# Optimization experiments

Measured on AMD Instinct MI355X. Metric: run time of the kernel, lower is better.

The kernel has to match this reference:

```python
import jax, jax.numpy as jnp
import numpy as np

N = 10000
E = 320000
DIM_IN, DIM_H, DIM_OUT, HEADS = 256, 64, 32, 8
NEG_SLOPE = 0.2


def setup_inputs() -> dict:
    key = jax.random.key(0)
    ks = jax.random.split(key, 10)
    x = jax.random.normal(ks[0], (N, DIM_IN), dtype=jnp.float32)
    edge_index = jax.random.randint(ks[1], (2, E), 0, N, dtype=jnp.int64)
    def glorot(k, shape, fan_in):
        return jax.random.normal(k, shape, dtype=jnp.float32) / np.sqrt(fan_in)
    # layer 1: GATv2Conv(256 -> 64, heads=8)
    W1l = glorot(ks[2], (DIM_IN, HEADS * DIM_H), DIM_IN)
    W1r = glorot(ks[3], (DIM_IN, HEADS * DIM_H), DIM_IN)
    att1 = glorot(ks[4], (HEADS, DIM_H), DIM_H)
    b1 = jnp.zeros((HEADS * DIM_H,), dtype=jnp.float32)
    # layer 2: GATv2Conv(512 -> 32, heads=1)
    W2l = glorot(ks[5], (HEADS * DIM_H, DIM_OUT), HEADS * DIM_H)
    W2r = glorot(ks[6], (HEADS * DIM_H, DIM_OUT), HEADS * DIM_H)
    att2 = glorot(ks[7], (1, DIM_OUT), DIM_OUT)
    b2 = jnp.zeros((DIM_OUT,), dtype=jnp.float32)
    return {"x": x, "edge_index": edge_index, "W1l": W1l, "W1r": W1r,
            "att1": att1, "b1": b1, "W2l": W2l, "W2r": W2r, "att2": att2, "b2": b2}


def gatv2_conv(x, src, dst, Wl, Wr, att, bias, heads, out_ch, concat):
    n = x.shape[0]
    xl = (x @ Wl).reshape(n, heads, out_ch)  # source transform
    xr = (x @ Wr).reshape(n, heads, out_ch)  # target transform
    e = jax.nn.leaky_relu(xl[src] + xr[dst], NEG_SLOPE)       # [E,H,C]
    alpha = jnp.einsum('ehc,hc->eh', e, att)                  # [E,H]
    amax = jax.lax.stop_gradient(
        jax.ops.segment_max(alpha, dst, num_segments=n))      # [N,H]
    ex = jnp.exp(alpha - amax[dst])
    denom = jax.ops.segment_sum(ex, dst, num_segments=n)
    alpha = ex / (denom[dst] + 1e-16)
    msg = xl[src] * alpha[..., None]                          # [E,H,C]
    out = jax.ops.segment_sum(msg, dst, num_segments=n)       # [N,H,C]
    out = out.reshape(n, heads * out_ch) if concat else out.mean(axis=1)
    return out + bias


def reference(x, edge_index, W1l, W1r, att1, b1, W2l, W2r, att2, b2):
    n = x.shape[0]
    loops = jnp.arange(n, dtype=edge_index.dtype)
    src = jnp.concatenate([edge_index[0], loops])  # add_self_loops=True (PyG default)
    dst = jnp.concatenate([edge_index[1], loops])
    h = gatv2_conv(x, src, dst, W1l, W1r, att1, b1, HEADS, DIM_H, True)
    h = jax.nn.elu(h)
    h = gatv2_conv(h, src, dst, W2l, W2r, att2, b2, 1, DIM_OUT, True)
    return jax.nn.log_softmax(h, axis=1)
```

## Files before the change

### kernel.cpp

```cpp
#include <hip/hip_runtime.h>
#include <hip/hip_bf16.h>


constexpr int N_NODES = 10000;
constexpr int N_EDGES = 320000;
constexpr int ET      = N_EDGES + N_NODES;
constexpr float NEG_SLOPE = 0.2f;

constexpr int NB_COUNT  = (ET + 255) / 256;
constexpr int NB_CONVX  = (N_NODES * 64) / 256;
constexpr int NB_CONVW  = (1024 * 64) / 256;
constexpr int NB_CONVW2 = (64 * 128) / 256;

typedef __attribute__((ext_vector_type(8))) short short8;
typedef __attribute__((ext_vector_type(8))) unsigned short ushort8_t;
typedef __attribute__((ext_vector_type(4))) float floatx4;

__device__ __forceinline__ float lrelu(float a) {
    return fmaxf(a, NEG_SLOPE * a);
}
__device__ __forceinline__ unsigned short f2bf(float f) {
    unsigned u = __float_as_uint(f);
    unsigned r = u + 0x7FFFu + ((u >> 16) & 1u);
    return (unsigned short)(r >> 16);
}
__device__ __forceinline__ float bf2f(unsigned short h) {
    return __uint_as_float((unsigned)h << 16);
}
__device__ __forceinline__ float red8_dpp(float p) {
    int x;
    x = __builtin_amdgcn_update_dpp(0, __float_as_int(p), 0xB1, 0xF, 0xF, true);
    p += __int_as_float(x);
    x = __builtin_amdgcn_update_dpp(0, __float_as_int(p), 0x4E, 0xF, 0xF, true);
    p += __int_as_float(x);
    x = __builtin_amdgcn_update_dpp(0, __float_as_int(p), 0x141, 0xF, 0xF, true);
    p += __int_as_float(x);
    return p;
}
__device__ __forceinline__ float red8max_dpp(float p) {
    int x;
    x = __builtin_amdgcn_update_dpp(0, __float_as_int(p), 0xB1, 0xF, 0xF, true);
    p = fmaxf(p, __int_as_float(x));
    x = __builtin_amdgcn_update_dpp(0, __float_as_int(p), 0x4E, 0xF, 0xF, true);
    p = fmaxf(p, __int_as_float(x));
    x = __builtin_amdgcn_update_dpp(0, __float_as_int(p), 0x141, 0xF, 0xF, true);
    p = fmaxf(p, __int_as_float(x));
    return p;
}
__device__ __forceinline__ float ror8_add(float p) {
    int x = __builtin_amdgcn_update_dpp(0, __float_as_int(p), 0x128, 0xF, 0xF, true);
    return p + __int_as_float(x);
}


__global__ __launch_bounds__(256) void k_prep(const int* __restrict__ ei,
        int* __restrict__ deg, const float* __restrict__ x,
        unsigned short* __restrict__ A, const float* __restrict__ Wl,
        const float* __restrict__ Wr, unsigned short* __restrict__ Bt,
        const float* __restrict__ W2l, const float* __restrict__ W2r,
        unsigned short* __restrict__ Bt2) {
    int b = blockIdx.x, t = threadIdx.x;
    if (b < NB_COUNT) {
        int e = b * 256 + t;
        if (e >= ET) return;
        int d = (e < N_EDGES) ? ei[N_EDGES + e] : (e - N_EDGES);
        atomicAdd(&deg[d], 1);
    } else if (b < NB_COUNT + NB_CONVX) {
        int idx = (b - NB_COUNT) * 256 + t;
        int m = idx >> 6, kg = (idx & 63) << 2;
        float4 v = *reinterpret_cast<const float4*>(x + (size_t)m * 256 + kg);
        ushort4 hi = make_ushort4(f2bf(v.x), f2bf(v.y), f2bf(v.z), f2bf(v.w));
        *reinterpret_cast<ushort4*>(A + (size_t)m * 256 + kg) = hi;
    } else if (b < NB_COUNT + NB_CONVX + NB_CONVW) {
        int idx = (b - NB_COUNT - NB_CONVX) * 256 + t;
        int n = idx >> 6, kg = (idx & 63) << 2;
        const float* src = (n < 512) ? (Wl + n) : (Wr + (n - 512));
        float v0 = src[(size_t)(kg + 0) * 512];
        float v1 = src[(size_t)(kg + 1) * 512];
        float v2 = src[(size_t)(kg + 2) * 512];
        float v3 = src[(size_t)(kg + 3) * 512];
        ushort4 hi = make_ushort4(f2bf(v0), f2bf(v1), f2bf(v2), f2bf(v3));
        *reinterpret_cast<ushort4*>(Bt + (size_t)n * 256 + kg) = hi;
    } else {
        int idx = (b - NB_COUNT - NB_CONVX - NB_CONVW) * 256 + t;
        int j = idx >> 7, kg = (idx & 127) << 2;
        const float* src = (j < 32) ? (W2l + j) : (W2r + (j - 32));
        float v0 = src[(size_t)(kg + 0) * 32];
        float v1 = src[(size_t)(kg + 1) * 32];
        float v2 = src[(size_t)(kg + 2) * 32];
        float v3 = src[(size_t)(kg + 3) * 32];
        ushort4 hi = make_ushort4(f2bf(v0), f2bf(v1), f2bf(v2), f2bf(v3));
        *reinterpret_cast<ushort4*>(Bt2 + (size_t)j * 512 + kg) = hi;
    }
}


__global__ __launch_bounds__(1024) void k_scan(const int* __restrict__ deg,
                                               int* __restrict__ offs) {
    __shared__ int part[1024];
    const int CH = 10;
    int t = threadIdx.x;
    int base = t * CH;
    int loc[CH];
    int s = 0;
    for (int i = 0; i < CH; ++i) {
        int idx = base + i;
        int v = (idx < N_NODES) ? deg[idx] : 0;
        loc[i] = s; s += v;
    }
    part[t] = s;
    __syncthreads();
    for (int o = 1; o < 1024; o <<= 1) {
        int add = (t >= o) ? part[t - o] : 0;
        __syncthreads();
        part[t] += add;
        __syncthreads();
    }
    int excl = part[t] - s;
    for (int i = 0; i < CH; ++i) {
        int idx = base + i;
        if (idx < N_NODES) offs[idx] = excl + loc[i];
    }
    if (t == 1023) offs[N_NODES] = part[1023];
}

__global__ void k_scatter(const int* __restrict__ ei, const int* __restrict__ offs,
                          int* __restrict__ deg, int* __restrict__ ssrc) {
    int e = blockIdx.x * 256 + threadIdx.x;
    if (e >= ET) return;
    int s, d;
    if (e < N_EDGES) { s = ei[e]; d = ei[N_EDGES + e]; }
    else             { s = d = e - N_EDGES; }
    int pos = offs[d] + atomicAdd(&deg[d], -1) - 1;
    ssrc[pos] = s;
}


__global__ __launch_bounds__(256) void k_mfma1(const unsigned short* __restrict__ A,
        const unsigned short* __restrict__ Bt, unsigned short* __restrict__ xl1b,
        unsigned short* __restrict__ xr1b) {
    __shared__ unsigned short As[128 * 40];
    __shared__ unsigned short Bs[128 * 40];
    int t = threadIdx.x;
    int wave = t >> 6, L = t & 63;
    int wm = wave & 1, wn = wave >> 1;
    int row0 = blockIdx.x * 128, n0 = blockIdx.y * 128;
    int q = L >> 4, rr = L & 15;
    floatx4 acc[4][4];
#pragma unroll
    for (int i = 0; i < 4; ++i)
#pragma unroll
        for (int j = 0; j < 4; ++j) acc[i][j] = (floatx4){0.f, 0.f, 0.f, 0.f};
    int ra = t >> 2,        ka = (t & 3) * 8;
    int rb = (t + 256) >> 2, kb = ((t + 256) & 3) * 8;
    int gma = row0 + ra; gma = (gma < N_NODES) ? gma : (N_NODES - 1);
    int gmb = row0 + rb; gmb = (gmb < N_NODES) ? gmb : (N_NODES - 1);
    for (int kc = 0; kc < 256; kc += 32) {
        __syncthreads();
        *reinterpret_cast<uint4*>(&As[ra * 40 + ka]) =
            *reinterpret_cast<const uint4*>(A + (size_t)gma * 256 + kc + ka);
        *reinterpret_cast<uint4*>(&As[rb * 40 + kb]) =
            *reinterpret_cast<const uint4*>(A + (size_t)gmb * 256 + kc + kb);
        *reinterpret_cast<uint4*>(&Bs[ra * 40 + ka]) =
            *reinterpret_cast<const uint4*>(Bt + (size_t)(n0 + ra) * 256 + kc + ka);
        *reinterpret_cast<uint4*>(&Bs[rb * 40 + kb]) =
            *reinterpret_cast<const uint4*>(Bt + (size_t)(n0 + rb) * 256 + kc + kb);
        __syncthreads();
        short8 af[4], bf[4];
#pragma unroll
        for (int st = 0; st < 4; ++st)
            af[st] = *reinterpret_cast<const short8*>(
                &As[(wm * 64 + st * 16 + rr) * 40 + q * 8]);
#pragma unroll
        for (int st = 0; st < 4; ++st)
            bf[st] = *reinterpret_cast<const short8*>(
                &Bs[(wn * 64 + st * 16 + rr) * 40 + q * 8]);
#pragma unroll
        for (int i = 0; i < 4; ++i)
#pragma unroll
            for (int j = 0; j < 4; ++j)
                acc[i][j] = __builtin_amdgcn_mfma_f32_16x16x32_bf16(
                    af[i], bf[j], acc[i][j], 0, 0, 0);
    }
#pragma unroll
    for (int j = 0; j < 4; ++j) {
        int gc = n0 + wn * 64 + j * 16 + rr;
        unsigned short* dst = (gc < 512) ? xl1b : xr1b;
        int col = (gc < 512) ? gc : (gc - 512);
#pragma unroll
        for (int i = 0; i < 4; ++i)
#pragma unroll
            for (int r = 0; r < 4; ++r) {
                int gr = row0 + wm * 64 + i * 16 + q * 4 + r;
                if (gr < N_NODES)
                    dst[(size_t)gr * 512 + col] = f2bf(acc[i][j][r]);
            }
    }
}

__global__ __launch_bounds__(256) void k_node1f(const int* __restrict__ offs,
        const int* __restrict__ ssrc, const unsigned short* __restrict__ xl1b,
        const unsigned short* __restrict__ xr1b, const float* __restrict__ att1,
        const float* __restrict__ b1, unsigned short* __restrict__ h1b) {
    int t = threadIdx.x;
    int wave = t >> 6, lane = t & 63;
    int n = blockIdx.x * 4 + wave;
    if (n >= N_NODES) return;
    int beg = offs[n], dcnt = offs[n + 1] - beg;
    float xrv[8], atv[8];
    {
        ushort8_t xru = *reinterpret_cast<const ushort8_t*>(
            xr1b + (size_t)n * 512 + lane * 8);
        const float* atrow = att1 + lane * 8;
        float4 c0 = *reinterpret_cast<const float4*>(atrow);
        float4 c1 = *reinterpret_cast<const float4*>(atrow + 4);
#pragma unroll
        for (int i = 0; i < 8; ++i) xrv[i] = bf2f(xru[i]);
        atv[0]=c0.x; atv[1]=c0.y; atv[2]=c0.z; atv[3]=c0.w;
        atv[4]=c1.x; atv[5]=c1.y; atv[6]=c1.z; atv[7]=c1.w;
    }
    float l = 0.f;
    float acc8[8];
#pragma unroll
    for (int i = 0; i < 8; ++i) acc8[i] = 0.f;
    const int* sp = ssrc + beg;
    const char* xlbase = reinterpret_cast<const char*>(xl1b) + lane * 16;
    auto ld_row = [&](int off) -> ushort8_t {
        return *reinterpret_cast<const ushort8_t*>(xlbase + off);
    };
    for (int b0 = 0; b0 < dcnt; b0 += 64) {
        int bn = dcnt - b0; if (bn > 64) bn = 64;
        int idxv = sp[b0 + ((lane < bn) ? lane : (bn - 1))];
        auto off_at = [&](int k) -> int {
            int kc = (k < bn) ? k : (bn - 1);
            return __shfl(idxv, kc, 64) << 10;
        };
        auto edge = [&](ushort8_t u, int idx) {
            float xs[8];
#pragma unroll
            for (int j = 0; j < 8; ++j) xs[j] = bf2f(u[j]);
            float p0 = 0.f, p1 = 0.f;
#pragma unroll
            for (int j = 0; j < 4; ++j) {
                p0 += lrelu(xs[j] + xrv[j]) * atv[j];
                p1 += lrelu(xs[j + 4] + xrv[j + 4]) * atv[j + 4];
            }
            float p = red8_dpp(p0 + p1);
            float w = __expf(fminf(p, 60.f));
            if (idx >= bn) w = 0.f;
            l += w;
#pragma unroll
            for (int j = 0; j < 8; ++j) acc8[j] += w * xs[j];
        };
        ushort8_t u0 = ld_row(off_at(0));
        ushort8_t u1 = ld_row(off_at(1));
        ushort8_t u2 = ld_row(off_at(2));
        ushort8_t u3 = ld_row(off_at(3));
        for (int i = 0; i < bn; i += 4) {
            ushort8_t n0 = ld_row(off_at(i + 4));
            ushort8_t n1 = ld_row(off_at(i + 5));
            ushort8_t n2 = ld_row(off_at(i + 6));
            ushort8_t n3 = ld_row(off_at(i + 7));
            edge(u0, i);
            edge(u1, i + 1);
            edge(u2, i + 2);
            edge(u3, i + 3);
            u0 = n0; u1 = n1; u2 = n2; u3 = n3;
        }
    }
    float inv = 1.f / (l + 1e-16f);
    const float* brow = b1 + lane * 8;
    ushort8_t vout;
#pragma unroll
    for (int j = 0; j < 8; ++j) {
        float v = acc8[j] * inv + brow[j];
        v = (v > 0.f) ? v : (__expf(v) - 1.f);
        vout[j] = f2bf(v);
    }
    *reinterpret_cast<ushort8_t*>(h1b + (size_t)n * 512 + lane * 8) = vout;
}


__global__ __launch_bounds__(256) void k_mfma2(const unsigned short* __restrict__ h1b,
        const unsigned short* __restrict__ Bt2, float* __restrict__ xw2) {
    __shared__ unsigned short Hs[64 * 40];
    __shared__ unsigned short Ws[64 * 40];
    int t = threadIdx.x;
    int wave = t >> 6, L = t & 63;
    int row0 = blockIdx.x * 64;
    int q = L >> 4, rr = L & 15;
    floatx4 acc[4];
#pragma unroll
    for (int j = 0; j < 4; ++j) acc[j] = (floatx4){0.f, 0.f, 0.f, 0.f};
    int ra = t >> 2, ka = (t & 3) * 8;
    int gma = row0 + ra; gma = (gma < N_NODES) ? gma : (N_NODES - 1);
    for (int kc = 0; kc < 512; kc += 32) {
        __syncthreads();
        *reinterpret_cast<uint4*>(&Hs[ra * 40 + ka]) =
            *reinterpret_cast<const uint4*>(h1b + (size_t)gma * 512 + kc + ka);
        *reinterpret_cast<uint4*>(&Ws[ra * 40 + ka]) =
            *reinterpret_cast<const uint4*>(Bt2 + (size_t)ra * 512 + kc + ka);
        __syncthreads();
        short8 af = *reinterpret_cast<const short8*>(
            &Hs[(wave * 16 + rr) * 40 + q * 8]);
#pragma unroll
        for (int j = 0; j < 4; ++j) {
            short8 bf = *reinterpret_cast<const short8*>(
                &Ws[(j * 16 + rr) * 40 + q * 8]);
            acc[j] = __builtin_amdgcn_mfma_f32_16x16x32_bf16(af, bf, acc[j], 0, 0, 0);
        }
    }
#pragma unroll
    for (int j = 0; j < 4; ++j) {
        int gc = j * 16 + rr;
#pragma unroll
        for (int r = 0; r < 4; ++r) {
            int gr = row0 + wave * 16 + q * 4 + r;
            if (gr < N_NODES) xw2[(size_t)gr * 64 + gc] = acc[j][r];
        }
    }
}

__global__ __launch_bounds__(256) void k_node2f(const int* __restrict__ offs,
        const int* __restrict__ ssrc, const float* __restrict__ xw2,
        const float* __restrict__ att2, const float* __restrict__ b2,
        float* __restrict__ out) {
    int t = threadIdx.x;
    int wave = t >> 6, lane = t & 63;
    int n = blockIdx.x * 4 + wave;
    if (n >= N_NODES) return;
    int ej = lane >> 3;
    int cg = lane & 7;
    int beg = offs[n], dcnt = offs[n + 1] - beg;
    float4 xr = *reinterpret_cast<const float4*>(
                    xw2 + (size_t)n * 64 + 32 + cg * 4);
    float4 at = *reinterpret_cast<const float4*>(att2 + cg * 4);
    float l = 0.f;
    float4 ac = {0.f, 0.f, 0.f, 0.f};
    const int* sp = ssrc + beg;
    const char* xwbase = reinterpret_cast<const char*>(xw2) + cg * 16;
    auto ld_off = [&](int i1) -> int {
        int i1c = (i1 < dcnt) ? i1 : (dcnt - 1);
        return sp[i1c] << 8;
    };
    auto ld_row = [&](int off) -> float4 {
        return *reinterpret_cast<const float4*>(xwbase + off);
    };
    int full = dcnt & ~15;
    float4 uA = ld_row(ld_off(ej));
    float4 uB = ld_row(ld_off(8 + ej));
    int oA1 = ld_off(16 + ej), oB1 = ld_off(24 + ej);
    for (int base = 0; base < full; base += 16) {
        float4 uA1 = ld_row(oA1), uB1 = ld_row(oB1);
        int oA2 = ld_off(base + 32 + ej);
        int oB2 = ld_off(base + 40 + ej);
        float pA0 = lrelu(uA.x + xr.x) * at.x + lrelu(uA.z + xr.z) * at.z;
        float pA1 = lrelu(uA.y + xr.y) * at.y + lrelu(uA.w + xr.w) * at.w;
        float pB0 = lrelu(uB.x + xr.x) * at.x + lrelu(uB.z + xr.z) * at.z;
        float pB1 = lrelu(uB.y + xr.y) * at.y + lrelu(uB.w + xr.w) * at.w;
        float wA = __expf(fminf(red8_dpp(pA0 + pA1), 60.f));
        float wB = __expf(fminf(red8_dpp(pB0 + pB1), 60.f));
        l += wA + wB;
        ac.x += wA * uA.x + wB * uB.x;
        ac.y += wA * uA.y + wB * uB.y;
        ac.z += wA * uA.z + wB * uB.z;
        ac.w += wA * uA.w + wB * uB.w;
        uA = uA1; uB = uB1; oA1 = oA2; oB1 = oB2;
    }
    if (full < dcnt) {
        float pA0 = lrelu(uA.x + xr.x) * at.x + lrelu(uA.z + xr.z) * at.z;
        float pA1 = lrelu(uA.y + xr.y) * at.y + lrelu(uA.w + xr.w) * at.w;
        float pB0 = lrelu(uB.x + xr.x) * at.x + lrelu(uB.z + xr.z) * at.z;
        float pB1 = lrelu(uB.y + xr.y) * at.y + lrelu(uB.w + xr.w) * at.w;
        float pA = red8_dpp(pA0 + pA1);
        float pB = red8_dpp(pB0 + pB1);
        if (full + ej >= dcnt)     pA = -1e30f;
        if (full + 8 + ej >= dcnt) pB = -1e30f;
        float wA = __expf(fminf(pA, 60.f));
        float wB = __expf(fminf(pB, 60.f));
        l += wA + wB;
        ac.x += wA * uA.x + wB * uB.x;
        ac.y += wA * uA.y + wB * uB.y;
        ac.z += wA * uA.z + wB * uB.z;
        ac.w += wA * uA.w + wB * uB.w;
    }
    l = ror8_add(l); l += __shfl_xor(l, 16); l += __shfl_xor(l, 32);
    ac.x = ror8_add(ac.x); ac.x += __shfl_xor(ac.x, 16); ac.x += __shfl_xor(ac.x, 32);
    ac.y = ror8_add(ac.y); ac.y += __shfl_xor(ac.y, 16); ac.y += __shfl_xor(ac.y, 32);
    ac.z = ror8_add(ac.z); ac.z += __shfl_xor(ac.z, 16); ac.z += __shfl_xor(ac.z, 32);
    ac.w = ror8_add(ac.w); ac.w += __shfl_xor(ac.w, 16); ac.w += __shfl_xor(ac.w, 32);
    float inv = 1.f / (l + 1e-16f);
    float4 bb = *reinterpret_cast<const float4*>(b2 + cg * 4);
    float4 v;
    v.x = ac.x * inv + bb.x; v.y = ac.y * inv + bb.y;
    v.z = ac.z * inv + bb.z; v.w = ac.w * inv + bb.w;
    float mx = red8max_dpp(fmaxf(fmaxf(v.x, v.y), fmaxf(v.z, v.w)));
    float se = red8_dpp(__expf(v.x - mx) + __expf(v.y - mx)
                      + __expf(v.z - mx) + __expf(v.w - mx));
    float ls = __logf(se);
    v.x = v.x - mx - ls; v.y = v.y - mx - ls;
    v.z = v.z - mx - ls; v.w = v.w - mx - ls;
    if (ej == 0)
        *reinterpret_cast<float4*>(out + (size_t)n * 32 + cg * 4) = v;
}


extern "C" void kernel_launch(void* const* d_in, const int* in_sizes, int n_in,
                              void* d_out, int out_size, void* d_ws, size_t ws_size,
                              hipStream_t stream) {
    (void)in_sizes; (void)n_in; (void)out_size; (void)ws_size;
    const float* x    = (const float*)d_in[0];
    const int*   ei   = (const int*)d_in[1];
    const float* W1l  = (const float*)d_in[2];
    const float* W1r  = (const float*)d_in[3];
    const float* att1 = (const float*)d_in[4];
    const float* b1   = (const float*)d_in[5];
    const float* W2l  = (const float*)d_in[6];
    const float* W2r  = (const float*)d_in[7];
    const float* att2 = (const float*)d_in[8];
    const float* b2   = (const float*)d_in[9];
    float* outp = (float*)d_out;

    char* ws = (char*)d_ws;
    size_t o = 0;
    auto alloc = [&](size_t bytes) {
        char* p = ws + o;
        o = (o + bytes + 255) & ~(size_t)255;
        return p;
    };
    unsigned short* xl1b = (unsigned short*)alloc((size_t)N_NODES * 512 * 2);
    unsigned short* xr1b = (unsigned short*)alloc((size_t)N_NODES * 512 * 2);
    unsigned short* h1b  = (unsigned short*)alloc((size_t)N_NODES * 512 * 2);
    float* xw2    = (float*)alloc((size_t)N_NODES * 64 * 4);
    unsigned short* Abf = (unsigned short*)alloc((size_t)N_NODES * 256 * 2);
    unsigned short* Bbf = (unsigned short*)alloc((size_t)1024 * 256 * 2);
    unsigned short* Bt2 = (unsigned short*)alloc((size_t)64 * 512 * 2);
    int*   deg    = (int*)alloc((size_t)N_NODES * 4);
    int*   offs   = (int*)alloc((size_t)(N_NODES + 1) * 4);
    int*   ssrc   = (int*)alloc((size_t)ET * 4);

    hipMemsetAsync(deg, 0, (size_t)N_NODES * 4, stream);

    k_prep   <<<NB_COUNT + NB_CONVX + NB_CONVW + NB_CONVW2, 256, 0, stream>>>(
                 ei, deg, x, Abf, W1l, W1r, Bbf, W2l, W2r, Bt2);
    k_scan   <<<1,                    1024, 0, stream>>>(deg, offs);
    k_scatter<<<(ET + 255) / 256,      256, 0, stream>>>(ei, offs, deg, ssrc);
    k_mfma1  <<<dim3(79, 8),           256, 0, stream>>>(Abf, Bbf, xl1b, xr1b);
    k_node1f <<<(N_NODES + 3) / 4,     256, 0, stream>>>(offs, ssrc, xl1b, xr1b, att1, b1, h1b);
    k_mfma2  <<<(N_NODES + 63) / 64,   256, 0, stream>>>(h1b, Bt2, xw2);
    k_node2f <<<(N_NODES + 3) / 4,     256, 0, stream>>>(offs, ssrc, xw2, att2, b2, outp);
}
```

Before: 205.4 us.

## Fuse scatter into GEMM launch, split node edges across two waves, pack math

Merges the CSR scatter kernel into the first MFMA GEMM as extra blocks of one launch, which removes a launch and lets the two overlap. Layer-1 aggregation now splits each node's edge list across two waves and combines their partial sums through shared memory, which doubles parallelism per node. The leaky-relu dot product is rewritten as 0.6*x + 0.4*|x| using packed fp32 FMA/add inline asm. Layer-2 aggregation now loads source indices with one batched load and shuffles them across the wave, in 64-edge chunks. The cost is a block-wide syncthreads and shared-memory traffic per node, plus slightly different float rounding.

New measurement: 201.9 us. No clear change (-1.7%).

```diff
diff --git a/kernel.cpp b/kernel.cpp
--- a/kernel.cpp
+++ b/kernel.cpp
@@ -11,10 +11,12 @@
 constexpr int NB_CONVX  = (N_NODES * 64) / 256;
 constexpr int NB_CONVW  = (1024 * 64) / 256;
 constexpr int NB_CONVW2 = (64 * 128) / 256;
+constexpr int NB_M1     = 79 * 8;
 
 typedef __attribute__((ext_vector_type(8))) short short8;
 typedef __attribute__((ext_vector_type(8))) unsigned short ushort8_t;
 typedef __attribute__((ext_vector_type(4))) float floatx4;
+typedef __attribute__((ext_vector_type(2))) float floatx2;
 
 __device__ __forceinline__ float lrelu(float a) {
     return fmaxf(a, NEG_SLOPE * a);
@@ -26,6 +28,22 @@
 }
 __device__ __forceinline__ float bf2f(unsigned short h) {
     return __uint_as_float((unsigned)h << 16);
+}
+__device__ __forceinline__ floatx2 pk_add(floatx2 a, floatx2 b) {
+    floatx2 d;
+    asm("v_pk_add_f32 %0, %1, %2" : "=v"(d) : "v"(a), "v"(b));
+    return d;
+}
+__device__ __forceinline__ floatx2 pk_fma(floatx2 a, floatx2 b, floatx2 c) {
+    floatx2 d;
+    asm("v_pk_fma_f32 %0, %1, %2, %3" : "=v"(d) : "v"(a), "v"(b), "v"(c));
+    return d;
+}
+__device__ __forceinline__ floatx2 unpk(unsigned w) {
+    floatx2 r;
+    r.x = __uint_as_float(w << 16);
+    r.y = __uint_as_float(w & 0xffff0000u);
+    return r;
 }
 __device__ __forceinline__ float red8_dpp(float p) {
     int x;
@@ -124,27 +142,29 @@
     if (t == 1023) offs[N_NODES] = part[1023];
 }
 
-__global__ void k_scatter(const int* __restrict__ ei, const int* __restrict__ offs,
-                          int* __restrict__ deg, int* __restrict__ ssrc) {
-    int e = blockIdx.x * 256 + threadIdx.x;
-    if (e >= ET) return;
-    int s, d;
-    if (e < N_EDGES) { s = ei[e]; d = ei[N_EDGES + e]; }
-    else             { s = d = e - N_EDGES; }
-    int pos = offs[d] + atomicAdd(&deg[d], -1) - 1;
-    ssrc[pos] = s;
-}
-
-
-__global__ __launch_bounds__(256) void k_mfma1(const unsigned short* __restrict__ A,
+
+__global__ __launch_bounds__(256) void k_scm1(const int* __restrict__ ei,
+        const int* __restrict__ offs, int* __restrict__ deg,
+        int* __restrict__ ssrc, const unsigned short* __restrict__ A,
         const unsigned short* __restrict__ Bt, unsigned short* __restrict__ xl1b,
         unsigned short* __restrict__ xr1b) {
     __shared__ unsigned short As[128 * 40];
     __shared__ unsigned short Bs[128 * 40];
     int t = threadIdx.x;
+    if (blockIdx.x < NB_COUNT) {
+        int e = blockIdx.x * 256 + t;
+        if (e >= ET) return;
+        int s, d;
+        if (e < N_EDGES) { s = ei[e]; d = ei[N_EDGES + e]; }
+        else             { s = d = e - N_EDGES; }
+        int pos = offs[d] + atomicAdd(&deg[d], -1) - 1;
+        ssrc[pos] = s;
+        return;
+    }
+    int bb = blockIdx.x - NB_COUNT;
+    int row0 = (bb % 79) * 128, n0 = (bb / 79) * 128;
     int wave = t >> 6, L = t & 63;
     int wm = wave & 1, wn = wave >> 1;
-    int row0 = blockIdx.x * 128, n0 = blockIdx.y * 128;
     int q = L >> 4, rr = L & 15;
     floatx4 acc[4][4];
 #pragma unroll
@@ -202,27 +222,44 @@
         const int* __restrict__ ssrc, const unsigned short* __restrict__ xl1b,
         const unsigned short* __restrict__ xr1b, const float* __restrict__ att1,
         const float* __restrict__ b1, unsigned short* __restrict__ h1b) {
+    __shared__ float comb[2][64][9];
     int t = threadIdx.x;
     int wave = t >> 6, lane = t & 63;
-    int n = blockIdx.x * 4 + wave;
-    if (n >= N_NODES) return;
-    int beg = offs[n], dcnt = offs[n + 1] - beg;
-    float xrv[8], atv[8];
+    int ni = wave >> 1, wv = wave & 1;
+    int n = blockIdx.x * 2 + ni;
+    int beg0 = offs[n], d = offs[n + 1] - beg0;
+    int half = (d + 1) >> 1;
+    int beg = beg0 + (wv ? half : 0);
+    int dcnt = wv ? (d - half) : half;
+    floatx2 xrp0, xrp1, xrp2, xrp3;
+    floatx2 c1p0, c1p1, c1p2, c1p3;
+    floatx2 c2p0, c2p1, c2p2, c2p3;
+    float K0;
     {
         ushort8_t xru = *reinterpret_cast<const ushort8_t*>(
             xr1b + (size_t)n * 512 + lane * 8);
+        union { ushort8_t v; uint4 w; } cv; cv.v = xru;
+        xrp0 = unpk(cv.w.x); xrp1 = unpk(cv.w.y);
+        xrp2 = unpk(cv.w.z); xrp3 = unpk(cv.w.w);
         const float* atrow = att1 + lane * 8;
         float4 c0 = *reinterpret_cast<const float4*>(atrow);
         float4 c1 = *reinterpret_cast<const float4*>(atrow + 4);
-#pragma unroll
-        for (int i = 0; i < 8; ++i) xrv[i] = bf2f(xru[i]);
-        atv[0]=c0.x; atv[1]=c0.y; atv[2]=c0.z; atv[3]=c0.w;
-        atv[4]=c1.x; atv[5]=c1.y; atv[6]=c1.z; atv[7]=c1.w;
-    }
+        c1p0 = (floatx2){0.6f * c0.x, 0.6f * c0.y};
+        c1p1 = (floatx2){0.6f * c0.z, 0.6f * c0.w};
+        c1p2 = (floatx2){0.6f * c1.x, 0.6f * c1.y};
+        c1p3 = (floatx2){0.6f * c1.z, 0.6f * c1.w};
+        c2p0 = (floatx2){0.4f * c0.x, 0.4f * c0.y};
+        c2p1 = (floatx2){0.4f * c0.z, 0.4f * c0.w};
+        c2p2 = (floatx2){0.4f * c1.x, 0.4f * c1.y};
+        c2p3 = (floatx2){0.4f * c1.z, 0.4f * c1.w};
+        K0 = c1p0.x * xrp0.x + c1p0.y * xrp0.y
+           + c1p1.x * xrp1.x + c1p1.y * xrp1.y
+           + c1p2.x * xrp2.x + c1p2.y * xrp2.y
+           + c1p3.x * xrp3.x + c1p3.y * xrp3.y;
+    }
+    floatx2 k0p = (floatx2){K0, 0.f};
     float l = 0.f;
-    float acc8[8];
-#pragma unroll
-    for (int i = 0; i < 8; ++i) acc8[i] = 0.f;
+    floatx2 ac0 = {0.f, 0.f}, ac1 = {0.f, 0.f}, ac2 = {0.f, 0.f}, ac3 = {0.f, 0.f};
     const int* sp = ssrc + beg;
     const char* xlbase = reinterpret_cast<const char*>(xl1b) + lane * 16;
     auto ld_row = [&](int off) -> ushort8_t {
@@ -236,48 +273,77 @@
             return __shfl(idxv, kc, 64) << 10;
         };
         auto edge = [&](ushort8_t u, int idx) {
-            float xs[8];
-#pragma unroll
-            for (int j = 0; j < 8; ++j) xs[j] = bf2f(u[j]);
-            float p0 = 0.f, p1 = 0.f;
-#pragma unroll
-            for (int j = 0; j < 4; ++j) {
-                p0 += lrelu(xs[j] + xrv[j]) * atv[j];
-                p1 += lrelu(xs[j + 4] + xrv[j + 4]) * atv[j + 4];
-            }
-            float p = red8_dpp(p0 + p1);
+            union { ushort8_t v; uint4 w; } cv; cv.v = u;
+            floatx2 xs0 = unpk(cv.w.x), xs1 = unpk(cv.w.y),
+                    xs2 = unpk(cv.w.z), xs3 = unpk(cv.w.w);
+            floatx2 dd = pk_fma(xs0, c1p0, k0p);
+            dd = pk_fma(xs1, c1p1, dd);
+            dd = pk_fma(xs2, c1p2, dd);
+            dd = pk_fma(xs3, c1p3, dd);
+            floatx2 a0 = pk_add(xs0, xrp0);
+            floatx2 a1 = pk_add(xs1, xrp1);
+            floatx2 a2 = pk_add(xs2, xrp2);
+            floatx2 a3 = pk_add(xs3, xrp3);
+            a0.x = fabsf(a0.x); a0.y = fabsf(a0.y);
+            a1.x = fabsf(a1.x); a1.y = fabsf(a1.y);
+            a2.x = fabsf(a2.x); a2.y = fabsf(a2.y);
+            a3.x = fabsf(a3.x); a3.y = fabsf(a3.y);
+            dd = pk_fma(a0, c2p0, dd);
+            dd = pk_fma(a1, c2p1, dd);
+            dd = pk_fma(a2, c2p2, dd);
+            dd = pk_fma(a3, c2p3, dd);
+            float p = red8_dpp(dd.x + dd.y);
             float w = __expf(fminf(p, 60.f));
             if (idx >= bn) w = 0.f;
             l += w;
-#pragma unroll
-            for (int j = 0; j < 8; ++j) acc8[j] += w * xs[j];
+            floatx2 wp = (floatx2){w, w};
+            ac0 = pk_fma(xs0, wp, ac0);
+            ac1 = pk_fma(xs1, wp, ac1);
+            ac2 = pk_fma(xs2, wp, ac2);
+            ac3 = pk_fma(xs3, wp, ac3);
         };
         ushort8_t u0 = ld_row(off_at(0));
         ushort8_t u1 = ld_row(off_at(1));
         ushort8_t u2 = ld_row(off_at(2));
         ushort8_t u3 = ld_row(off_at(3));
         for (int i = 0; i < bn; i += 4) {
-            ushort8_t n0 = ld_row(off_at(i + 4));
-            ushort8_t n1 = ld_row(off_at(i + 5));
-            ushort8_t n2 = ld_row(off_at(i + 6));
-            ushort8_t n3 = ld_row(off_at(i + 7));
+            ushort8_t p0 = ld_row(off_at(i + 4));
+            ushort8_t p1 = ld_row(off_at(i + 5));
+            ushort8_t p2 = ld_row(off_at(i + 6));
+            ushort8_t p3 = ld_row(off_at(i + 7));
             edge(u0, i);
             edge(u1, i + 1);
             edge(u2, i + 2);
             edge(u3, i + 3);
-            u0 = n0; u1 = n1; u2 = n2; u3 = n3;
+            u0 = p0; u1 = p1; u2 = p2; u3 = p3;
         }
     }
-    float inv = 1.f / (l + 1e-16f);
-    const float* brow = b1 + lane * 8;
-    ushort8_t vout;
-#pragma unroll
-    for (int j = 0; j < 8; ++j) {
-        float v = acc8[j] * inv + brow[j];
-        v = (v > 0.f) ? v : (__expf(v) - 1.f);
-        vout[j] = f2bf(v);
-    }
-    *reinterpret_cast<ushort8_t*>(h1b + (size_t)n * 512 + lane * 8) = vout;
+    if (wv == 1) {
+        float* cb = &comb[ni][lane][0];
+        cb[0] = ac0.x; cb[1] = ac0.y; cb[2] = ac1.x; cb[3] = ac1.y;
+        cb[4] = ac2.x; cb[5] = ac2.y; cb[6] = ac3.x; cb[7] = ac3.y;
+        cb[8] = l;
+    }
+    __syncthreads();
+    if (wv == 0) {
+        const float* cb = &comb[ni][lane][0];
+        float av0 = ac0.x + cb[0], av1 = ac0.y + cb[1];
+        float av2 = ac1.x + cb[2], av3 = ac1.y + cb[3];
+        float av4 = ac2.x + cb[4], av5 = ac2.y + cb[5];
+        float av6 = ac3.x + cb[6], av7 = ac3.y + cb[7];
+        float lt = l + cb[8];
+        float inv = 1.f / (lt + 1e-16f);
+        const float* brow = b1 + lane * 8;
+        float av[8] = {av0, av1, av2, av3, av4, av5, av6, av7};
+        ushort8_t vout;
+#pragma unroll
+        for (int j = 0; j < 8; ++j) {
+            float v = av[j] * inv + brow[j];
+            v = (v > 0.f) ? v : (__expf(v) - 1.f);
+            vout[j] = f2bf(v);
+        }
+        *reinterpret_cast<ushort8_t*>(h1b + (size_t)n * 512 + lane * 8) = vout;
+    }
 }
 
 
@@ -339,50 +405,40 @@
     float4 ac = {0.f, 0.f, 0.f, 0.f};
     const int* sp = ssrc + beg;
     const char* xwbase = reinterpret_cast<const char*>(xw2) + cg * 16;
-    auto ld_off = [&](int i1) -> int {
-        int i1c = (i1 < dcnt) ? i1 : (dcnt - 1);
-        return sp[i1c] << 8;
-    };
     auto ld_row = [&](int off) -> float4 {
         return *reinterpret_cast<const float4*>(xwbase + off);
     };
-    int full = dcnt & ~15;
-    float4 uA = ld_row(ld_off(ej));
-    float4 uB = ld_row(ld_off(8 + ej));
-    int oA1 = ld_off(16 + ej), oB1 = ld_off(24 + ej);
-    for (int base = 0; base < full; base += 16) {
-        float4 uA1 = ld_row(oA1), uB1 = ld_row(oB1);
-        int oA2 = ld_off(base + 32 + ej);
-        int oB2 = ld_off(base + 40 + ej);
-        float pA0 = lrelu(uA.x + xr.x) * at.x + lrelu(uA.z + xr.z) * at.z;
-        float pA1 = lrelu(uA.y + xr.y) * at.y + lrelu(uA.w + xr.w) * at.w;
-        float pB0 = lrelu(uB.x + xr.x) * at.x + lrelu(uB.z + xr.z) * at.z;
-        float pB1 = lrelu(uB.y + xr.y) * at.y + lrelu(uB.w + xr.w) * at.w;
-        float wA = __expf(fminf(red8_dpp(pA0 + pA1), 60.f));
-        float wB = __expf(fminf(red8_dpp(pB0 + pB1), 60.f));
-        l += wA + wB;
-        ac.x += wA * uA.x + wB * uB.x;
-        ac.y += wA * uA.y + wB * uB.y;
-        ac.z += wA * uA.z + wB * uB.z;
-        ac.w += wA * uA.w + wB * uB.w;
-        uA = uA1; uB = uB1; oA1 = oA2; oB1 = oB2;
-    }
-    if (full < dcnt) {
-        float pA0 = lrelu(uA.x + xr.x) * at.x + lrelu(uA.z + xr.z) * at.z;
-        float pA1 = lrelu(uA.y + xr.y) * at.y + lrelu(uA.w + xr.w) * at.w;
-        float pB0 = lrelu(uB.x + xr.x) * at.x + lrelu(uB.z + xr.z) * at.z;
-        float pB1 = lrelu(uB.y + xr.y) * at.y + lrelu(uB.w + xr.w) * at.w;
-        float pA = red8_dpp(pA0 + pA1);
-        float pB = red8_dpp(pB0 + pB1);
-        if (full + ej >= dcnt)     pA = -1e30f;
-        if (full + 8 + ej >= dcnt) pB = -1e30f;
-        float wA = __expf(fminf(pA, 60.f));
-        float wB = __expf(fminf(pB, 60.f));
-        l += wA + wB;
-        ac.x += wA * uA.x + wB * uB.x;
-        ac.y += wA * uA.y + wB * uB.y;
-        ac.z += wA * uA.z + wB * uB.z;
-        ac.w += wA * uA.w + wB * uB.w;
+    for (int b0 = 0; b0 < dcnt; b0 += 64) {
+        int bn = dcnt - b0; if (bn > 64) bn = 64;
+        int idxv = sp[b0 + ((lane < bn) ? lane : (bn - 1))];
+        auto off_at = [&](int k) -> int {
+            int kc = (k < bn) ? k : (bn - 1);
+            return __shfl(idxv, kc, 64) << 8;
+        };
+        float4 uA  = ld_row(off_at(ej));
+        float4 uB  = ld_row(off_at(8 + ej));
+        float4 uA1 = ld_row(off_at(16 + ej));
+        float4 uB1 = ld_row(off_at(24 + ej));
+        for (int base = 0; base < bn; base += 16) {
+            float4 uA2 = ld_row(off_at(base + 32 + ej));
+            float4 uB2 = ld_row(off_at(base + 40 + ej));
+            float pA0 = lrelu(uA.x + xr.x) * at.x + lrelu(uA.z + xr.z) * at.z;
+            float pA1 = lrelu(uA.y + xr.y) * at.y + lrelu(uA.w + xr.w) * at.w;
+            float pB0 = lrelu(uB.x + xr.x) * at.x + lrelu(uB.z + xr.z) * at.z;
+            float pB1 = lrelu(uB.y + xr.y) * at.y + lrelu(uB.w + xr.w) * at.w;
+            float pA = red8_dpp(pA0 + pA1);
+            float pB = red8_dpp(pB0 + pB1);
+            if (base + ej >= bn)     pA = -1e30f;
+            if (base + 8 + ej >= bn) pB = -1e30f;
+            float wA = __expf(fminf(pA, 60.f));
+            float wB = __expf(fminf(pB, 60.f));
+            l += wA + wB;
+            ac.x += wA * uA.x + wB * uB.x;
+            ac.y += wA * uA.y + wB * uB.y;
+            ac.z += wA * uA.z + wB * uB.z;
+            ac.w += wA * uA.w + wB * uB.w;
+            uA = uA1; uB = uB1; uA1 = uA2; uB1 = uB2;
+        }
     }
     l = ror8_add(l); l += __shfl_xor(l, 16); l += __shfl_xor(l, 32);
     ac.x = ror8_add(ac.x); ac.x += __shfl_xor(ac.x, 16); ac.x += __shfl_xor(ac.x, 32);
@@ -444,9 +500,9 @@
     k_prep   <<<NB_COUNT + NB_CONVX + NB_CONVW + NB_CONVW2, 256, 0, stream>>>(
                  ei, deg, x, Abf, W1l, W1r, Bbf, W2l, W2r, Bt2);
     k_scan   <<<1,                    1024, 0, stream>>>(deg, offs);
-    k_scatter<<<(ET + 255) / 256,      256, 0, stream>>>(ei, offs, deg, ssrc);
-    k_mfma1  <<<dim3(79, 8),           256, 0, stream>>>(Abf, Bbf, xl1b, xr1b);
-    k_node1f <<<(N_NODES + 3) / 4,     256, 0, stream>>>(offs, ssrc, xl1b, xr1b, att1, b1, h1b);
+    k_scm1   <<<NB_COUNT + NB_M1,      256, 0, stream>>>(ei, offs, deg, ssrc,
+                                                         Abf, Bbf, xl1b, xr1b);
+    k_node1f <<<N_NODES / 2,           256, 0, stream>>>(offs, ssrc, xl1b, xr1b, att1, b1, h1b);
     k_mfma2  <<<(N_NODES + 63) / 64,   256, 0, stream>>>(h1b, Bt2, xw2);
     k_node2f <<<(N_NODES + 3) / 4,     256, 0, stream>>>(offs, ssrc, xw2, att2, b2, outp);
 }
```
